# Optimization experiments

Hardware: AMD Instinct MI355X
Metric: run time of the kernel (lower is better)

## Reference

```python
import jax, jax.numpy as jnp
import numpy as np
import math

B, S, E, H, R = 2, 2048, 1024, 16, 128
D = E // H  # head_dim = 64
EPS = 1e-5


def _ln(x, g, b):
    mu = jnp.mean(x, axis=-1, keepdims=True)
    var = jnp.mean((x - mu) ** 2, axis=-1, keepdims=True)
    return (x - mu) * jax.lax.rsqrt(var + EPS) * g + b


def setup_inputs() -> dict:
    key = jax.random.key(0)
    ks = jax.random.split(key, 16)
    f32 = jnp.float32
    inp = {
        "hidden_states": jax.random.normal(ks[0], (B, S, E), f32),
        # GPT2 Conv1D-style c_attn / c_proj: y = x @ W + b
        "w_attn": jax.random.normal(ks[1], (E, 3 * E), f32) * (0.02),
        "b_attn": jnp.zeros((3 * E,), f32),
        "w_proj": jax.random.normal(ks[2], (E, E), f32) * 0.02,
        "b_proj": jnp.zeros((E,), f32),
        # low-rank factors, stored as [in, out] so y = x @ W
        "qw1": jax.random.normal(ks[3], (D, R), f32) * 0.1,
        "qw2": jax.random.normal(ks[4], (D, R), f32) * 0.1,
        "kw3": jax.random.normal(ks[5], (D, R), f32) * 0.1,
        "kw4": jax.random.normal(ks[6], (D, R), f32) * 0.1,
        "qproj": jax.random.normal(ks[7], (R, D), f32) * 0.02,
        "kproj": jax.random.normal(ks[8], (R, D), f32) * 0.02,
        "alpha_q": jnp.zeros((1, H, 1, 1), f32),
        "alpha_k": jnp.zeros((1, H, 1, 1), f32),
        "temperature": jnp.ones((1, H, 1, 1), f32),
        "g_q": jnp.ones((D,), f32),
        "beta_q": jnp.zeros((D,), f32),
        "g_k": jnp.ones((D,), f32),
        "beta_k": jnp.zeros((D,), f32),
    }
    return inp


def reference(hidden_states, w_attn, b_attn, w_proj, b_proj, qw1, qw2, kw3, kw4,
              qproj, kproj, alpha_q, alpha_k, temperature, g_q, beta_q, g_k, beta_k):
    qkv = hidden_states @ w_attn + b_attn                       # [B,S,3E]
    q, k, v = jnp.split(qkv, 3, axis=-1)
    split = lambda t: t.reshape(B, S, H, D).transpose(0, 2, 1, 3)  # [B,H,S,D]
    q, k, v = split(q), split(k), split(v)

    qn = _ln(q, g_q, beta_q)
    kn = _ln(k, g_k, beta_k)

    # low-rank multiplicative interaction + GELU + projection back (dropout = eval/no-op)
    q_struct_raw = jax.nn.gelu((qn @ qw1) * (qn @ qw2), approximate=False) @ qproj
    k_struct_raw = jax.nn.gelu((kn @ kw3) * (kn @ kw4), approximate=False) @ kproj

    q_struct = q + jax.nn.sigmoid(alpha_q) * q_struct_raw
    k_struct = k + jax.nn.sigmoid(alpha_k) * k_struct_raw

    scores = jnp.einsum("bhqd,bhkd->bhqk", q_struct, k_struct)
    scores = scores / (math.sqrt(D) * temperature)

    causal = jnp.tril(jnp.ones((S, S), dtype=bool))
    scores = jnp.where(causal, scores, jnp.finfo(scores.dtype).min)

    attn = jax.nn.softmax(scores, axis=-1)                       # [B,H,S,S]
    out = jnp.einsum("bhqk,bhkd->bhqd", attn, v)
    out = out.transpose(0, 2, 1, 3).reshape(B, S, E)
    return out @ w_proj + b_proj
```

## Files before the change

kernel.cpp:

```cpp
#include <hip/hip_runtime.h>
#include <hip/hip_bf16.h>
#include <math.h>

#define B_ 2
#define S_ 2048
#define E_ 1024
#define H_ 16
#define D_ 64
#define R_ 128
#define EPS_ 1e-5f

typedef __bf16 bf16x8_t __attribute__((ext_vector_type(8)));
typedef float f32x4_t __attribute__((ext_vector_type(4)));

__device__ __forceinline__ float sigmoidf_(float x) {
  return 1.0f / (1.0f + __expf(-x));
}

__device__ __forceinline__ unsigned short f2bf(float f) {
  __hip_bfloat16 h = __float2bfloat16(f);
  return *reinterpret_cast<unsigned short*>(&h);
}

typedef const __attribute__((address_space(1))) unsigned int ga_u32_t;
typedef __attribute__((address_space(3))) unsigned int ls_u32_t;
__device__ __forceinline__ void gload_lds16(const void* g, void* l) {
  __builtin_amdgcn_global_load_lds((ga_u32_t*)g, (ls_u32_t*)l, 16, 0, 0);
}

__global__ __launch_bounds__(256) void cast_bf16(
    const float* __restrict__ in, unsigned short* __restrict__ out, int n4) {
  int i = blockIdx.x * 256 + threadIdx.x;
  if (i >= n4) return;
  float4 v = ((const float4*)in)[i];
  ushort4 o;
  o.x = f2bf(v.x); o.y = f2bf(v.y); o.z = f2bf(v.z); o.w = f2bf(v.w);
  ((ushort4*)out)[i] = o;
}

__global__ __launch_bounds__(256) void transpose_cast(
    const float* __restrict__ in, unsigned short* __restrict__ out,
    int K, int N) {
  __shared__ unsigned short t[64][65];
  const int k0 = blockIdx.y * 64, n0 = blockIdx.x * 64;
  for (int i = threadIdx.x; i < 64 * 64; i += 256) {
    int r = i >> 6, c = i & 63;
    t[c][r] = f2bf(in[(size_t)(k0 + r) * N + n0 + c]);
  }
  __syncthreads();
  for (int i = threadIdx.x; i < 64 * 64; i += 256) {
    int r = i >> 6, c = i & 63;
    out[(size_t)(n0 + r) * K + k0 + c] = t[r][c];
  }
}

__global__ __launch_bounds__(256) void prep_weights(
    const float* __restrict__ qw1, const float* __restrict__ qw2,
    const float* __restrict__ kw3, const float* __restrict__ kw4,
    const float* __restrict__ qproj, const float* __restrict__ kproj,
    unsigned short* __restrict__ qw1T, unsigned short* __restrict__ qw2T,
    unsigned short* __restrict__ kw3T, unsigned short* __restrict__ kw4T,
    unsigned short* __restrict__ qprojT, unsigned short* __restrict__ kprojT) {
  __shared__ unsigned short t[64][65];
  const int which = blockIdx.x >> 1, half = blockIdx.x & 1;
  const float* in; unsigned short* out; int K, N, k0, n0;
  if (which < 4) {
    const float* ins[4] = {qw1, qw2, kw3, kw4};
    unsigned short* outs[4] = {qw1T, qw2T, kw3T, kw4T};
    in = ins[which]; out = outs[which]; K = 64; N = 128; k0 = 0; n0 = half * 64;
  } else {
    in = (which == 4) ? qproj : kproj;
    out = (which == 4) ? qprojT : kprojT;
    K = 128; N = 64; k0 = half * 64; n0 = 0;
  }
  for (int i = threadIdx.x; i < 64 * 64; i += 256) {
    int r = i >> 6, c = i & 63;
    t[c][r] = f2bf(in[(size_t)(k0 + r) * N + n0 + c]);
  }
  __syncthreads();
  for (int i = threadIdx.x; i < 64 * 64; i += 256) {
    int r = i >> 6, c = i & 63;
    out[(size_t)(n0 + r) * K + k0 + c] = t[r][c];
  }
}

__global__ __launch_bounds__(256) void fa_gemm_bf16(
    const unsigned short* __restrict__ A,
    const unsigned short* __restrict__ BT,
    const float* __restrict__ bias, float* __restrict__ C,
    int M, int N, int K) {
  __shared__ __align__(16) unsigned short Al[4][128][8];
  __shared__ __align__(16) unsigned short Bl[4][128][8];
  const int tid = threadIdx.x;
  const int w = tid >> 6, lane = tid & 63, lr = lane & 15, lg = lane >> 4;
  const int wm = w >> 1, wn = w & 1;
  const int row0 = blockIdx.y * 128, col0 = blockIdx.x * 128;

  f32x4_t acc[4][4];
  #pragma unroll
  for (int mf = 0; mf < 4; ++mf)
    #pragma unroll
    for (int nf = 0; nf < 4; ++nf) acc[mf][nf] = {0.f, 0.f, 0.f, 0.f};

  for (int k0 = 0; k0 < K; k0 += 32) {
    __syncthreads();
    #pragma unroll
    for (int it = 0; it < 2; ++it) {
      const int Lb = w * 128 + it * 64;
      const int kblk = Lb >> 7, rbase = Lb & 127;
      gload_lds16(A + (size_t)(row0 + rbase + lane) * K + k0 + kblk * 8,
                  (char*)Al + (size_t)Lb * 16);
      gload_lds16(BT + (size_t)(col0 + rbase + lane) * K + k0 + kblk * 8,
                  (char*)Bl + (size_t)Lb * 16);
    }
    __syncthreads();

    bf16x8_t af[4], bfr[4];
    #pragma unroll
    for (int mf = 0; mf < 4; ++mf)
      af[mf] = *(const bf16x8_t*)&Al[lg][wm * 64 + mf * 16 + lr][0];
    #pragma unroll
    for (int nf = 0; nf < 4; ++nf)
      bfr[nf] = *(const bf16x8_t*)&Bl[lg][wn * 64 + nf * 16 + lr][0];
    #pragma unroll
    for (int mf = 0; mf < 4; ++mf)
      #pragma unroll
      for (int nf = 0; nf < 4; ++nf)
        acc[mf][nf] = __builtin_amdgcn_mfma_f32_16x16x32_bf16(
            af[mf], bfr[nf], acc[mf][nf], 0, 0, 0);
  }

  #pragma unroll
  for (int mf = 0; mf < 4; ++mf)
    #pragma unroll
    for (int nf = 0; nf < 4; ++nf) {
      const int col = col0 + wn * 64 + nf * 16 + lr;
      const float bv = bias[col];
      #pragma unroll
      for (int j = 0; j < 4; ++j) {
        const int row = row0 + wm * 64 + mf * 16 + lg * 4 + j;
        C[(size_t)row * N + col] = acc[mf][nf][j] + bv;
      }
    }
}

__global__ __launch_bounds__(256) void fa_struct_mfma(
    const float* __restrict__ qkv,
    const unsigned short* __restrict__ qw1T, const unsigned short* __restrict__ qw2T,
    const unsigned short* __restrict__ kw3T, const unsigned short* __restrict__ kw4T,
    const unsigned short* __restrict__ qprojT, const unsigned short* __restrict__ kprojT,
    const float* __restrict__ alpha_q, const float* __restrict__ alpha_k,
    const float* __restrict__ temperature,
    const float* __restrict__ g_q, const float* __restrict__ beta_q,
    const float* __restrict__ g_k, const float* __restrict__ beta_k,
    unsigned short* __restrict__ q_struct, unsigned short* __restrict__ k_struct,
    unsigned short* __restrict__ v_t) {
  __shared__ __align__(16) char smem[49152];
  const int bx = blockIdx.x;
  const int bh = bx >> 4, s0 = (bx & 15) * 128;
  const int b = bh >> 4, h = bh & 15;
  const int tid = threadIdx.x, wv = tid >> 6, lane = tid & 63;
  const int lr = lane & 15, lg = lane >> 4;
  const int r0 = wv * 32;
  char* const xn = smem + wv * 4096;
  char* const gl = smem + 16384 + wv * 8192;

  {
    unsigned short* vlds = (unsigned short*)(smem + 16384);
    const int s = tid >> 1, dh = tid & 1;
    const float* src = qkv + ((size_t)b * S_ + s0 + s) * (3 * E_) + 2 * E_ +
                       h * 64 + dh * 32;
    #pragma unroll
    for (int i = 0; i < 32; i += 4) {
      float4 v4 = *(const float4*)(src + i);
      vlds[(dh * 32 + i + 0) * 136 + s] = f2bf(v4.x);
      vlds[(dh * 32 + i + 1) * 136 + s] = f2bf(v4.y);
      vlds[(dh * 32 + i + 2) * 136 + s] = f2bf(v4.z);
      vlds[(dh * 32 + i + 3) * 136 + s] = f2bf(v4.w);
    }
    __syncthreads();
    const int d = tid >> 2, qt = tid & 3;
    unsigned short* dst = v_t + ((size_t)bh * 64 + d) * S_ + s0 + qt * 32;
    const unsigned short* srow = vlds + d * 136 + qt * 32;
    #pragma unroll
    for (int i = 0; i < 32; i += 8)
      *(uint4*)(dst + i) = *(const uint4*)(srow + i);
    __syncthreads();
  }

  const float qscale = 1.4426950408889634f / (8.0f * temperature[h]);
  const float sgq = sigmoidf_(alpha_q[h]);
  const float sgk = sigmoidf_(alpha_k[h]);

  auto process = [&](const unsigned short* w1T, const unsigned short* w2T,
                     const unsigned short* wPT, const float* gvec,
                     const float* bvec, int qkoff, float sg, float oscale,
                     unsigned short* outp) {
    {
      const int rrow = lane >> 2, sub = lane & 3;
      float gv[16], bv[16];
      #pragma unroll
      for (int i = 0; i < 16; i += 4) {
        *(float4*)(gv + i) = *(const float4*)(gvec + sub * 16 + i);
        *(float4*)(bv + i) = *(const float4*)(bvec + sub * 16 + i);
      }
      #pragma unroll
      for (int pass = 0; pass < 2; ++pass) {
        const int row = pass * 16 + rrow;
        const float* src = qkv + ((size_t)b * S_ + s0 + r0 + row) * (3 * E_) +
                           qkoff + h * 64 + sub * 16;
        float x[16];
        #pragma unroll
        for (int i = 0; i < 16; i += 4) *(float4*)(x + i) = *(const float4*)(src + i);
        float sm = 0.f;
        #pragma unroll
        for (int i = 0; i < 16; ++i) sm += x[i];
        sm += __shfl_xor(sm, 1, 64);
        sm += __shfl_xor(sm, 2, 64);
        const float mu = sm * (1.0f / 64.0f);
        float v2 = 0.f;
        #pragma unroll
        for (int i = 0; i < 16; ++i) { float dd = x[i] - mu; v2 += dd * dd; }
        v2 += __shfl_xor(v2, 1, 64);
        v2 += __shfl_xor(v2, 2, 64);
        const float rs = rsqrtf(v2 * (1.0f / 64.0f) + EPS_);
        unsigned short xb[16];
        #pragma unroll
        for (int i = 0; i < 16; ++i)
          xb[i] = f2bf((x[i] - mu) * rs * gv[i] + bv[i]);
        const int sw = (row & 7) << 4;
        *(uint4*)(xn + ((row * 128 + sub * 32) ^ sw)) = *(uint4*)(xb);
        *(uint4*)(xn + ((row * 128 + sub * 32 + 16) ^ sw)) = *(uint4*)(xb + 8);
      }
    }

    bf16x8_t a[2][2];
    #pragma unroll
    for (int mf = 0; mf < 2; ++mf)
      #pragma unroll
      for (int ks = 0; ks < 2; ++ks) {
        const int row = mf * 16 + lr;
        a[mf][ks] = *(const bf16x8_t*)(xn +
            ((row * 128 + ks * 64 + lg * 16) ^ ((row & 7) << 4)));
      }
    #pragma unroll
    for (int nf = 0; nf < 8; ++nf) {
      f32x4_t t1[2] = {{0.f,0.f,0.f,0.f},{0.f,0.f,0.f,0.f}};
      f32x4_t t2[2] = {{0.f,0.f,0.f,0.f},{0.f,0.f,0.f,0.f}};
      #pragma unroll
      for (int ks = 0; ks < 2; ++ks) {
        bf16x8_t b1 = *(const bf16x8_t*)(w1T + (size_t)(nf * 16 + lr) * 64 +
                                         ks * 32 + lg * 8);
        bf16x8_t b2 = *(const bf16x8_t*)(w2T + (size_t)(nf * 16 + lr) * 64 +
                                         ks * 32 + lg * 8);
        #pragma unroll
        for (int mf = 0; mf < 2; ++mf) {
          t1[mf] = __builtin_amdgcn_mfma_f32_16x16x32_bf16(a[mf][ks], b1, t1[mf], 0, 0, 0);
          t2[mf] = __builtin_amdgcn_mfma_f32_16x16x32_bf16(a[mf][ks], b2, t2[mf], 0, 0, 0);
        }
      }
      #pragma unroll
      for (int mf = 0; mf < 2; ++mf)
        #pragma unroll
        for (int j = 0; j < 4; ++j) {
          const float xg = t1[mf][j] * t2[mf][j];
          const float ge = 0.5f * xg * (1.0f + erff(xg * 0.70710678118654752f));
          const int row = mf * 16 + lg * 4 + j;
          const int n = nf * 16 + lr;
          *(__bf16*)(gl + ((row * 256 + n * 2) ^ ((row & 7) << 4))) = (__bf16)ge;
        }
    }

    f32x4_t acc[2][4];
    #pragma unroll
    for (int mf = 0; mf < 2; ++mf)
      #pragma unroll
      for (int nf2 = 0; nf2 < 4; ++nf2) acc[mf][nf2] = {0.f, 0.f, 0.f, 0.f};
    #pragma unroll
    for (int ks2 = 0; ks2 < 4; ++ks2) {
      bf16x8_t pa[2];
      #pragma unroll
      for (int mf = 0; mf < 2; ++mf) {
        const int row = mf * 16 + lr;
        pa[mf] = *(const bf16x8_t*)(gl +
            ((row * 256 + ks2 * 64 + lg * 16) ^ ((row & 7) << 4)));
      }
      #pragma unroll
      for (int nf2 = 0; nf2 < 4; ++nf2) {
        bf16x8_t bP = *(const bf16x8_t*)(wPT + (size_t)(nf2 * 16 + lr) * 128 +
                                         ks2 * 32 + lg * 8);
        #pragma unroll
        for (int mf = 0; mf < 2; ++mf)
          acc[mf][nf2] = __builtin_amdgcn_mfma_f32_16x16x32_bf16(
              pa[mf], bP, acc[mf][nf2], 0, 0, 0);
      }
    }

    #pragma unroll
    for (int mf = 0; mf < 2; ++mf)
      #pragma unroll
      for (int nf2 = 0; nf2 < 4; ++nf2) {
        const int d = nf2 * 16 + lr;
        #pragma unroll
        for (int j = 0; j < 4; ++j) {
          const int srow = s0 + r0 + mf * 16 + lg * 4 + j;
          const float raw =
              qkv[((size_t)b * S_ + srow) * (3 * E_) + qkoff + h * 64 + d];
          outp[((size_t)bh * S_ + srow) * 64 + d] =
              f2bf((raw + sg * acc[mf][nf2][j]) * oscale);
        }
      }
  };

  process(qw1T, qw2T, qprojT, g_q, beta_q, 0, sgq, qscale, q_struct);
  process(kw3T, kw4T, kprojT, g_k, beta_k, E_, sgk, 1.0f, k_struct);
}

__global__ __launch_bounds__(256, 2) void fa_flash_mfma(
    const unsigned short* __restrict__ q_s,
    const unsigned short* __restrict__ k_s,
    const unsigned short* __restrict__ v_t,
    unsigned short* __restrict__ attn_out) {
  __shared__ __align__(16) unsigned short Kl[2][64][64];
  __shared__ __align__(16) unsigned short Vl[2][64][64];
  __shared__ __align__(16) char plds[4 * 2048];

  const int n = blockIdx.x;
  const int bh = (n & 7) + 8 * ((n >> 3) & 3);
  const int p = n >> 5;
  const int b = bh >> 4, h = bh & 15;
  const int tid = threadIdx.x;
  const int w = tid >> 6, lane = tid & 63;
  const int lr = lane & 15, lg = lane >> 4;
  char* const pw = plds + w * 2048;

  auto stage = [&](int buf, int kt) {
    const int s_base = kt * 64;
    #pragma unroll
    for (int r = 0; r < 2; ++r) {
      const int idx = tid + r * 256;
      const int row = idx >> 3;
      const int ck = (idx & 7) ^ (row & 7);
      gload_lds16(k_s + ((size_t)bh * S_ + s_base + row) * 64 + ck * 8,
                  (char*)Kl + buf * 8192 + idx * 16);
      gload_lds16(v_t + ((size_t)bh * 64 + row) * S_ + s_base + ck * 8,
                  (char*)Vl + buf * 8192 + idx * 16);
    }
  };

  auto run_tile = [&](int qt) {
    const int qrow0 = qt * 64 + w * 16;

    bf16x8_t aQ[2];
    #pragma unroll
    for (int ks = 0; ks < 2; ++ks)
      aQ[ks] = __builtin_bit_cast(bf16x8_t,
          *(const uint4*)(q_s + ((size_t)bh * S_ + qrow0 + lr) * 64 +
                          ks * 32 + lg * 8));

    f32x4_t O[4];
    float mrow[4], lrow[4];
    #pragma unroll
    for (int nf = 0; nf < 4; ++nf) O[nf] = {0.f, 0.f, 0.f, 0.f};
    #pragma unroll
    for (int r = 0; r < 4; ++r) { mrow[r] = -INFINITY; lrow[r] = 0.f; }

    stage(0, 0);
    __syncthreads();

    int buf = 0;
    for (int kt = 0; kt <= qt; ++kt) {
      if (kt < qt) stage(buf ^ 1, kt + 1);

      const char* Kb = (const char*)Kl + buf * 8192;
      const char* Vb = (const char*)Vl + buf * 8192;

      f32x4_t S[4];
      #pragma unroll
      for (int nf = 0; nf < 4; ++nf) S[nf] = {0.f, 0.f, 0.f, 0.f};
      #pragma unroll
      for (int ks = 0; ks < 2; ++ks)
        #pragma unroll
        for (int nf = 0; nf < 4; ++nf) {
          const int row = nf * 16 + lr;
          bf16x8_t bK = *(const bf16x8_t*)(Kb +
              ((row * 128 + ks * 64 + lg * 16) ^ ((row & 7) << 4)));
          S[nf] = __builtin_amdgcn_mfma_f32_16x16x32_bf16(
              aQ[ks], bK, S[nf], 0, 0, 0);
        }

      if (kt == qt) {
        #pragma unroll
        for (int nf = 0; nf < 4; ++nf)
          #pragma unroll
          for (int r = 0; r < 4; ++r) {
            int row = qrow0 + lg * 4 + r;
            int col = kt * 64 + nf * 16 + lr;
            if (col > row) S[nf][r] = -INFINITY;
          }
      }

      #pragma unroll
      for (int r = 0; r < 4; ++r) {
        float tmax = fmaxf(fmaxf(S[0][r], S[1][r]), fmaxf(S[2][r], S[3][r]));
        tmax = fmaxf(tmax, __shfl_xor(tmax, 1, 64));
        tmax = fmaxf(tmax, __shfl_xor(tmax, 2, 64));
        tmax = fmaxf(tmax, __shfl_xor(tmax, 4, 64));
        tmax = fmaxf(tmax, __shfl_xor(tmax, 8, 64));
        float mnew = fmaxf(mrow[r], tmax);
        float al = exp2f(mrow[r] - mnew);
        mrow[r] = mnew;
        const int rr = lg * 4 + r;
        char* rbase = pw + rr * 128;
        const int sw = (rr & 7) << 4;
        float psum = 0.f;
        #pragma unroll
        for (int nf = 0; nf < 4; ++nf) {
          float pv = exp2f(S[nf][r] - mnew);
          psum += pv;
          *(__bf16*)(rbase + (((nf * 16 + lr) * 2) ^ sw)) = (__bf16)pv;
        }
        lrow[r] = lrow[r] * al + psum;
        #pragma unroll
        for (int nf = 0; nf < 4; ++nf) O[nf][r] *= al;
      }

      #pragma unroll
      for (int ks2 = 0; ks2 < 2; ++ks2) {
        const int rr2 = lr;
        bf16x8_t pa = __builtin_bit_cast(bf16x8_t,
            *(const uint4*)(pw + rr2 * 128 +
                            ((ks2 * 64 + lg * 16) ^ ((rr2 & 7) << 4))));
        #pragma unroll
        for (int nf2 = 0; nf2 < 4; ++nf2) {
          const int drow = nf2 * 16 + lr;
          bf16x8_t bV = *(const bf16x8_t*)(Vb +
              ((drow * 128 + ks2 * 64 + lg * 16) ^ ((drow & 7) << 4)));
          O[nf2] = __builtin_amdgcn_mfma_f32_16x16x32_bf16(
              pa, bV, O[nf2], 0, 0, 0);
        }
      }

      __syncthreads();
      buf ^= 1;
    }

    #pragma unroll
    for (int r = 0; r < 4; ++r) {
      float l = lrow[r];
      l += __shfl_xor(l, 1, 64);
      l += __shfl_xor(l, 2, 64);
      l += __shfl_xor(l, 4, 64);
      l += __shfl_xor(l, 8, 64);
      float inv = 1.0f / l;
      int srow = qrow0 + lg * 4 + r;
      unsigned short* orow = attn_out + ((size_t)b * S_ + srow) * E_ + h * 64;
      #pragma unroll
      for (int nf = 0; nf < 4; ++nf)
        orow[nf * 16 + lr] = f2bf(O[nf][r] * inv);
    }
  };

  run_tile(p);
  run_tile(31 - p);
}

extern "C" void kernel_launch(void* const* d_in, const int* in_sizes, int n_in,
                              void* d_out, int out_size, void* d_ws, size_t ws_size,
                              hipStream_t stream) {
  const float* hidden = (const float*)d_in[0];
  const float* w_attn = (const float*)d_in[1];
  const float* b_attn = (const float*)d_in[2];
  const float* w_proj = (const float*)d_in[3];
  const float* b_proj = (const float*)d_in[4];
  const float* qw1    = (const float*)d_in[5];
  const float* qw2    = (const float*)d_in[6];
  const float* kw3    = (const float*)d_in[7];
  const float* kw4    = (const float*)d_in[8];
  const float* qproj  = (const float*)d_in[9];
  const float* kproj  = (const float*)d_in[10];
  const float* alpha_q = (const float*)d_in[11];
  const float* alpha_k = (const float*)d_in[12];
  const float* temperature = (const float*)d_in[13];
  const float* g_q    = (const float*)d_in[14];
  const float* beta_q = (const float*)d_in[15];
  const float* g_k    = (const float*)d_in[16];
  const float* beta_k = (const float*)d_in[17];
  float* out = (float*)d_out;

  const size_t QKV_ELEMS  = (size_t)B_ * S_ * 3 * E_;
  const size_t HEAD_ELEMS = (size_t)B_ * H_ * S_ * D_;
  const size_t HID_ELEMS  = (size_t)B_ * S_ * E_;

  float* ws = (float*)d_ws;
  float* qkv = ws;
  unsigned short* us = (unsigned short*)(ws + QKV_ELEMS);
  unsigned short* q_s = us;
  unsigned short* k_s = q_s + HEAD_ELEMS;
  unsigned short* v_t = k_s + HEAD_ELEMS;
  unsigned short* hbf = v_t + HEAD_ELEMS;
  unsigned short* wTa = hbf + HID_ELEMS;
  unsigned short* wTp = wTa + (size_t)E_ * 3 * E_;
  unsigned short* lw  = wTp + (size_t)E_ * E_;
  unsigned short* qw1T = lw;
  unsigned short* qw2T = qw1T + 8192;
  unsigned short* kw3T = qw2T + 8192;
  unsigned short* kw4T = kw3T + 8192;
  unsigned short* qprojT = kw4T + 8192;
  unsigned short* kprojT = qprojT + 8192;
  unsigned short* attn_bf = (unsigned short*)ws;

  const int nh4 = (int)(HID_ELEMS / 4);
  cast_bf16<<<(nh4 + 255) / 256, 256, 0, stream>>>(hidden, hbf, nh4);
  transpose_cast<<<dim3(3 * E_ / 64, E_ / 64), 256, 0, stream>>>(
      w_attn, wTa, E_, 3 * E_);
  transpose_cast<<<dim3(E_ / 64, E_ / 64), 256, 0, stream>>>(
      w_proj, wTp, E_, E_);
  prep_weights<<<dim3(12), 256, 0, stream>>>(
      qw1, qw2, kw3, kw4, qproj, kproj, qw1T, qw2T, kw3T, kw4T, qprojT, kprojT);

  fa_gemm_bf16<<<dim3(3 * E_ / 128, B_ * S_ / 128), 256, 0, stream>>>(
      hbf, wTa, b_attn, qkv, B_ * S_, 3 * E_, E_);

  fa_struct_mfma<<<dim3(512), 256, 0, stream>>>(
      qkv, qw1T, qw2T, kw3T, kw4T, qprojT, kprojT, alpha_q, alpha_k,
      temperature, g_q, beta_q, g_k, beta_k, q_s, k_s, v_t);

  fa_flash_mfma<<<dim3(512), 256, 0, stream>>>(q_s, k_s, v_t, attn_bf);

  fa_gemm_bf16<<<dim3(E_ / 128, B_ * S_ / 128), 256, 0, stream>>>(
      attn_bf, wTp, b_proj, out, B_ * S_, E_, E_);
}
```

Before: 338.8 us.

## Split struct kernel into Q and K waves with smaller tiles and LDS residual

The struct kernel now launches twice as many blocks, each covering 64 sequence rows instead of 128. Waves 0-1 handle Q and waves 2-3 handle K in parallel, replacing the old sequential Q-then-K pass in every wave. The raw q/k values are kept in registers, written to LDS as bf16, and read back for the residual add instead of being re-read from global fp32. This should raise parallelism and cut global traffic, at the cost of rounding the residual term to bf16 before the add.

```diff
diff --git a/kernel.cpp b/kernel.cpp
--- a/kernel.cpp
+++ b/kernel.cpp
@@ -157,163 +157,178 @@
     unsigned short* __restrict__ v_t) {
   __shared__ __align__(16) char smem[49152];
   const int bx = blockIdx.x;
-  const int bh = bx >> 4, s0 = (bx & 15) * 128;
+  const int bh = bx >> 5, s0 = (bx & 31) * 64;
   const int b = bh >> 4, h = bh & 15;
   const int tid = threadIdx.x, wv = tid >> 6, lane = tid & 63;
   const int lr = lane & 15, lg = lane >> 4;
-  const int r0 = wv * 32;
+  const bool isq = wv < 2;
+  const int r0 = (wv & 1) * 32;
   char* const xn = smem + wv * 4096;
   char* const gl = smem + 16384 + wv * 8192;
 
   {
     unsigned short* vlds = (unsigned short*)(smem + 16384);
-    const int s = tid >> 1, dh = tid & 1;
+    const int s = tid >> 2, dq = tid & 3;
     const float* src = qkv + ((size_t)b * S_ + s0 + s) * (3 * E_) + 2 * E_ +
-                       h * 64 + dh * 32;
-    #pragma unroll
-    for (int i = 0; i < 32; i += 4) {
+                       h * 64 + dq * 16;
+    #pragma unroll
+    for (int i = 0; i < 16; i += 4) {
       float4 v4 = *(const float4*)(src + i);
-      vlds[(dh * 32 + i + 0) * 136 + s] = f2bf(v4.x);
-      vlds[(dh * 32 + i + 1) * 136 + s] = f2bf(v4.y);
-      vlds[(dh * 32 + i + 2) * 136 + s] = f2bf(v4.z);
-      vlds[(dh * 32 + i + 3) * 136 + s] = f2bf(v4.w);
+      vlds[(dq * 16 + i + 0) * 72 + s] = f2bf(v4.x);
+      vlds[(dq * 16 + i + 1) * 72 + s] = f2bf(v4.y);
+      vlds[(dq * 16 + i + 2) * 72 + s] = f2bf(v4.z);
+      vlds[(dq * 16 + i + 3) * 72 + s] = f2bf(v4.w);
     }
     __syncthreads();
     const int d = tid >> 2, qt = tid & 3;
-    unsigned short* dst = v_t + ((size_t)bh * 64 + d) * S_ + s0 + qt * 32;
-    const unsigned short* srow = vlds + d * 136 + qt * 32;
-    #pragma unroll
-    for (int i = 0; i < 32; i += 8)
-      *(uint4*)(dst + i) = *(const uint4*)(srow + i);
+    unsigned short* dst = v_t + ((size_t)bh * 64 + d) * S_ + s0 + qt * 16;
+    const unsigned short* srow = vlds + d * 72 + qt * 16;
+    *(uint4*)(dst + 0) = *(const uint4*)(srow + 0);
+    *(uint4*)(dst + 8) = *(const uint4*)(srow + 8);
     __syncthreads();
   }
 
-  const float qscale = 1.4426950408889634f / (8.0f * temperature[h]);
-  const float sgq = sigmoidf_(alpha_q[h]);
-  const float sgk = sigmoidf_(alpha_k[h]);
-
-  auto process = [&](const unsigned short* w1T, const unsigned short* w2T,
-                     const unsigned short* wPT, const float* gvec,
-                     const float* bvec, int qkoff, float sg, float oscale,
-                     unsigned short* outp) {
-    {
-      const int rrow = lane >> 2, sub = lane & 3;
-      float gv[16], bv[16];
-      #pragma unroll
-      for (int i = 0; i < 16; i += 4) {
-        *(float4*)(gv + i) = *(const float4*)(gvec + sub * 16 + i);
-        *(float4*)(bv + i) = *(const float4*)(bvec + sub * 16 + i);
-      }
-      #pragma unroll
-      for (int pass = 0; pass < 2; ++pass) {
-        const int row = pass * 16 + rrow;
-        const float* src = qkv + ((size_t)b * S_ + s0 + r0 + row) * (3 * E_) +
-                           qkoff + h * 64 + sub * 16;
-        float x[16];
-        #pragma unroll
-        for (int i = 0; i < 16; i += 4) *(float4*)(x + i) = *(const float4*)(src + i);
-        float sm = 0.f;
-        #pragma unroll
-        for (int i = 0; i < 16; ++i) sm += x[i];
-        sm += __shfl_xor(sm, 1, 64);
-        sm += __shfl_xor(sm, 2, 64);
-        const float mu = sm * (1.0f / 64.0f);
-        float v2 = 0.f;
-        #pragma unroll
-        for (int i = 0; i < 16; ++i) { float dd = x[i] - mu; v2 += dd * dd; }
-        v2 += __shfl_xor(v2, 1, 64);
-        v2 += __shfl_xor(v2, 2, 64);
-        const float rs = rsqrtf(v2 * (1.0f / 64.0f) + EPS_);
-        unsigned short xb[16];
-        #pragma unroll
-        for (int i = 0; i < 16; ++i)
-          xb[i] = f2bf((x[i] - mu) * rs * gv[i] + bv[i]);
-        const int sw = (row & 7) << 4;
-        *(uint4*)(xn + ((row * 128 + sub * 32) ^ sw)) = *(uint4*)(xb);
-        *(uint4*)(xn + ((row * 128 + sub * 32 + 16) ^ sw)) = *(uint4*)(xb + 8);
-      }
-    }
-
-    bf16x8_t a[2][2];
+  const int qkoff = isq ? 0 : E_;
+  const unsigned short* w1T = isq ? qw1T : kw3T;
+  const unsigned short* w2T = isq ? qw2T : kw4T;
+  const unsigned short* wPT = isq ? qprojT : kprojT;
+  const float* gvec = isq ? g_q : g_k;
+  const float* bvec = isq ? beta_q : beta_k;
+  const float sg = sigmoidf_(isq ? alpha_q[h] : alpha_k[h]);
+  const float oscale =
+      isq ? (1.4426950408889634f / (8.0f * temperature[h])) : 1.0f;
+  unsigned short* outp = isq ? q_struct : k_struct;
+
+  float xr[2][16];
+  {
+    const int rrow = lane >> 2, sub = lane & 3;
+    float gv[16], bv[16];
+    #pragma unroll
+    for (int i = 0; i < 16; i += 4) {
+      *(float4*)(gv + i) = *(const float4*)(gvec + sub * 16 + i);
+      *(float4*)(bv + i) = *(const float4*)(bvec + sub * 16 + i);
+    }
+    #pragma unroll
+    for (int pass = 0; pass < 2; ++pass) {
+      const int row = pass * 16 + rrow;
+      const float* src = qkv + ((size_t)b * S_ + s0 + r0 + row) * (3 * E_) +
+                         qkoff + h * 64 + sub * 16;
+      float* x = xr[pass];
+      #pragma unroll
+      for (int i = 0; i < 16; i += 4) *(float4*)(x + i) = *(const float4*)(src + i);
+      float sm = 0.f;
+      #pragma unroll
+      for (int i = 0; i < 16; ++i) sm += x[i];
+      sm += __shfl_xor(sm, 1, 64);
+      sm += __shfl_xor(sm, 2, 64);
+      const float mu = sm * (1.0f / 64.0f);
+      float v2 = 0.f;
+      #pragma unroll
+      for (int i = 0; i < 16; ++i) { float dd = x[i] - mu; v2 += dd * dd; }
+      v2 += __shfl_xor(v2, 1, 64);
+      v2 += __shfl_xor(v2, 2, 64);
+      const float rs = rsqrtf(v2 * (1.0f / 64.0f) + EPS_);
+      unsigned short xb[16];
+      #pragma unroll
+      for (int i = 0; i < 16; ++i)
+        xb[i] = f2bf((x[i] - mu) * rs * gv[i] + bv[i]);
+      const int sw = (row & 7) << 4;
+      *(uint4*)(xn + ((row * 128 + sub * 32) ^ sw)) = *(uint4*)(xb);
+      *(uint4*)(xn + ((row * 128 + sub * 32 + 16) ^ sw)) = *(uint4*)(xb + 8);
+    }
+  }
+
+  bf16x8_t a[2][2];
+  #pragma unroll
+  for (int mf = 0; mf < 2; ++mf)
+    #pragma unroll
+    for (int ks = 0; ks < 2; ++ks) {
+      const int row = mf * 16 + lr;
+      a[mf][ks] = *(const bf16x8_t*)(xn +
+          ((row * 128 + ks * 64 + lg * 16) ^ ((row & 7) << 4)));
+    }
+  {
+    const int rrow = lane >> 2, sub = lane & 3;
+    #pragma unroll
+    for (int pass = 0; pass < 2; ++pass) {
+      const int row = pass * 16 + rrow;
+      unsigned short rb[16];
+      #pragma unroll
+      for (int i = 0; i < 16; ++i) rb[i] = f2bf(xr[pass][i]);
+      const int sw = (row & 7) << 4;
+      *(uint4*)(xn + ((row * 128 + sub * 32) ^ sw)) = *(uint4*)(rb);
+      *(uint4*)(xn + ((row * 128 + sub * 32 + 16) ^ sw)) = *(uint4*)(rb + 8);
+    }
+  }
+
+  #pragma unroll
+  for (int nf = 0; nf < 8; ++nf) {
+    f32x4_t t1[2] = {{0.f,0.f,0.f,0.f},{0.f,0.f,0.f,0.f}};
+    f32x4_t t2[2] = {{0.f,0.f,0.f,0.f},{0.f,0.f,0.f,0.f}};
+    #pragma unroll
+    for (int ks = 0; ks < 2; ++ks) {
+      bf16x8_t b1 = *(const bf16x8_t*)(w1T + (size_t)(nf * 16 + lr) * 64 +
+                                       ks * 32 + lg * 8);
+      bf16x8_t b2 = *(const bf16x8_t*)(w2T + (size_t)(nf * 16 + lr) * 64 +
+                                       ks * 32 + lg * 8);
+      #pragma unroll
+      for (int mf = 0; mf < 2; ++mf) {
+        t1[mf] = __builtin_amdgcn_mfma_f32_16x16x32_bf16(a[mf][ks], b1, t1[mf], 0, 0, 0);
+        t2[mf] = __builtin_amdgcn_mfma_f32_16x16x32_bf16(a[mf][ks], b2, t2[mf], 0, 0, 0);
+      }
+    }
     #pragma unroll
     for (int mf = 0; mf < 2; ++mf)
       #pragma unroll
-      for (int ks = 0; ks < 2; ++ks) {
-        const int row = mf * 16 + lr;
-        a[mf][ks] = *(const bf16x8_t*)(xn +
-            ((row * 128 + ks * 64 + lg * 16) ^ ((row & 7) << 4)));
-      }
-    #pragma unroll
-    for (int nf = 0; nf < 8; ++nf) {
-      f32x4_t t1[2] = {{0.f,0.f,0.f,0.f},{0.f,0.f,0.f,0.f}};
-      f32x4_t t2[2] = {{0.f,0.f,0.f,0.f},{0.f,0.f,0.f,0.f}};
-      #pragma unroll
-      for (int ks = 0; ks < 2; ++ks) {
-        bf16x8_t b1 = *(const bf16x8_t*)(w1T + (size_t)(nf * 16 + lr) * 64 +
-                                         ks * 32 + lg * 8);
-        bf16x8_t b2 = *(const bf16x8_t*)(w2T + (size_t)(nf * 16 + lr) * 64 +
-                                         ks * 32 + lg * 8);
-        #pragma unroll
-        for (int mf = 0; mf < 2; ++mf) {
-          t1[mf] = __builtin_amdgcn_mfma_f32_16x16x32_bf16(a[mf][ks], b1, t1[mf], 0, 0, 0);
-          t2[mf] = __builtin_amdgcn_mfma_f32_16x16x32_bf16(a[mf][ks], b2, t2[mf], 0, 0, 0);
-        }
-      }
+      for (int j = 0; j < 4; ++j) {
+        const float xg = t1[mf][j] * t2[mf][j];
+        const float ge = 0.5f * xg * (1.0f + erff(xg * 0.70710678118654752f));
+        const int row = mf * 16 + lg * 4 + j;
+        const int n = nf * 16 + lr;
+        *(__bf16*)(gl + ((row * 256 + n * 2) ^ ((row & 7) << 4))) = (__bf16)ge;
+      }
+  }
+
+  f32x4_t acc[2][4];
+  #pragma unroll
+  for (int mf = 0; mf < 2; ++mf)
+    #pragma unroll
+    for (int nf2 = 0; nf2 < 4; ++nf2) acc[mf][nf2] = {0.f, 0.f, 0.f, 0.f};
+  #pragma unroll
+  for (int ks2 = 0; ks2 < 4; ++ks2) {
+    bf16x8_t pa[2];
+    #pragma unroll
+    for (int mf = 0; mf < 2; ++mf) {
+      const int row = mf * 16 + lr;
+      pa[mf] = *(const bf16x8_t*)(gl +
+          ((row * 256 + ks2 * 64 + lg * 16) ^ ((row & 7) << 4)));
+    }
+    #pragma unroll
+    for (int nf2 = 0; nf2 < 4; ++nf2) {
+      bf16x8_t bP = *(const bf16x8_t*)(wPT + (size_t)(nf2 * 16 + lr) * 128 +
+                                       ks2 * 32 + lg * 8);
       #pragma unroll
       for (int mf = 0; mf < 2; ++mf)
-        #pragma unroll
-        for (int j = 0; j < 4; ++j) {
-          const float xg = t1[mf][j] * t2[mf][j];
-          const float ge = 0.5f * xg * (1.0f + erff(xg * 0.70710678118654752f));
-          const int row = mf * 16 + lg * 4 + j;
-          const int n = nf * 16 + lr;
-          *(__bf16*)(gl + ((row * 256 + n * 2) ^ ((row & 7) << 4))) = (__bf16)ge;
-        }
-    }
-
-    f32x4_t acc[2][4];
-    #pragma unroll
-    for (int mf = 0; mf < 2; ++mf)
-      #pragma unroll
-      for (int nf2 = 0; nf2 < 4; ++nf2) acc[mf][nf2] = {0.f, 0.f, 0.f, 0.f};
-    #pragma unroll
-    for (int ks2 = 0; ks2 < 4; ++ks2) {
-      bf16x8_t pa[2];
-      #pragma unroll
-      for (int mf = 0; mf < 2; ++mf) {
-        const int row = mf * 16 + lr;
-        pa[mf] = *(const bf16x8_t*)(gl +
-            ((row * 256 + ks2 * 64 + lg * 16) ^ ((row & 7) << 4)));
-      }
-      #pragma unroll
-      for (int nf2 = 0; nf2 < 4; ++nf2) {
-        bf16x8_t bP = *(const bf16x8_t*)(wPT + (size_t)(nf2 * 16 + lr) * 128 +
-                                         ks2 * 32 + lg * 8);
-        #pragma unroll
-        for (int mf = 0; mf < 2; ++mf)
-          acc[mf][nf2] = __builtin_amdgcn_mfma_f32_16x16x32_bf16(
-              pa[mf], bP, acc[mf][nf2], 0, 0, 0);
-      }
-    }
-
-    #pragma unroll
-    for (int mf = 0; mf < 2; ++mf)
-      #pragma unroll
-      for (int nf2 = 0; nf2 < 4; ++nf2) {
-        const int d = nf2 * 16 + lr;
-        #pragma unroll
-        for (int j = 0; j < 4; ++j) {
-          const int srow = s0 + r0 + mf * 16 + lg * 4 + j;
-          const float raw =
-              qkv[((size_t)b * S_ + srow) * (3 * E_) + qkoff + h * 64 + d];
-          outp[((size_t)bh * S_ + srow) * 64 + d] =
-              f2bf((raw + sg * acc[mf][nf2][j]) * oscale);
-        }
-      }
-  };
-
-  process(qw1T, qw2T, qprojT, g_q, beta_q, 0, sgq, qscale, q_struct);
-  process(kw3T, kw4T, kprojT, g_k, beta_k, E_, sgk, 1.0f, k_struct);
+        acc[mf][nf2] = __builtin_amdgcn_mfma_f32_16x16x32_bf16(
+            pa[mf], bP, acc[mf][nf2], 0, 0, 0);
+    }
+  }
+
+  #pragma unroll
+  for (int mf = 0; mf < 2; ++mf)
+    #pragma unroll
+    for (int nf2 = 0; nf2 < 4; ++nf2) {
+      const int d = nf2 * 16 + lr;
+      #pragma unroll
+      for (int j = 0; j < 4; ++j) {
+        const int row = mf * 16 + lg * 4 + j;
+        const float raw = (float)*(const __bf16*)(xn +
+            ((row * 128 + d * 2) ^ ((row & 7) << 4)));
+        const int srow = s0 + r0 + row;
+        outp[((size_t)bh * S_ + srow) * 64 + d] =
+            f2bf((raw + sg * acc[mf][nf2][j]) * oscale);
+      }
+    }
 }
 
 __global__ __launch_bounds__(256, 2) void fa_flash_mfma(
@@ -522,7 +537,7 @@
   fa_gemm_bf16<<<dim3(3 * E_ / 128, B_ * S_ / 128), 256, 0, stream>>>(
       hbf, wTa, b_attn, qkv, B_ * S_, 3 * E_, E_);
 
-  fa_struct_mfma<<<dim3(512), 256, 0, stream>>>(
+  fa_struct_mfma<<<dim3(1024), 256, 0, stream>>>(
       qkv, qw1T, qw2T, kw3T, kw4T, qprojT, kprojT, alpha_q, alpha_k,
       temperature, g_q, beta_q, g_k, beta_k, q_s, k_s, v_t);
 
```

Measured after the change: 310.3 us. -8.4%, faster.
